# Kernel tuning notes

Measured on AMD Instinct MI355X. Metric: run time of the kernel, lower is better.

## Reference

```python
import jax, jax.numpy as jnp
import numpy as np

NUM_HEADS = 16
BLOCK_SIZE = 64
NUM_GLOBAL_TOKENS = 64
WINDOW_SIZE = 256
NUM_RANDOM_BLOCKS = 3
BATCH = 2
SEQ_LEN = 4096
EMBED_DIM = 1024


def _alibi_slopes(n):
    # power-of-2 head count path of _compute_alibi_slopes
    base = 2.0 ** (-(2.0 ** (-(np.log2(n) - 3.0))))
    return jnp.asarray([base ** i for i in range(1, n + 1)], dtype=jnp.float32)


def _build_block_indices():
    nb = SEQ_LEN // BLOCK_SIZE
    ngb = NUM_GLOBAL_TOKENS // BLOCK_SIZE
    wb = WINDOW_SIZE // BLOCK_SIZE
    mb = 2 * wb + 1 + NUM_RANDOM_BLOCKS
    rng = np.random.default_rng(0)
    out = np.full((nb, mb), -1, dtype=np.int64)
    for qb in range(nb):
        attended = set(range(ngb))  # global blocks handled separately
        idx = 0
        for kb in range(max(ngb, qb - wb), min(nb, qb + wb + 1)):
            if kb not in attended:
                out[qb, idx] = kb
                attended.add(kb)
                idx += 1
        cand = [b for b in range(ngb, nb) if b not in attended]
        pick = rng.choice(len(cand), size=min(NUM_RANDOM_BLOCKS, len(cand)), replace=False)
        for j in pick:
            out[qb, idx] = cand[j]
            idx += 1
    return jnp.asarray(out)


def setup_inputs() -> dict:
    key = jax.random.key(0)
    ks = jax.random.split(key, 5)
    s = 0.02
    x = jax.random.normal(ks[0], (BATCH, SEQ_LEN, EMBED_DIM), jnp.float32)
    Wq = jax.random.normal(ks[1], (EMBED_DIM, EMBED_DIM), jnp.float32) * s
    Wk = jax.random.normal(ks[2], (EMBED_DIM, EMBED_DIM), jnp.float32) * s
    Wv = jax.random.normal(ks[3], (EMBED_DIM, EMBED_DIM), jnp.float32) * s
    Wo = jax.random.normal(ks[4], (EMBED_DIM, EMBED_DIM), jnp.float32) * s
    return {"x": x, "Wq": Wq, "Wk": Wk, "Wv": Wv, "Wo": Wo,
            "block_indices": _build_block_indices()}


def reference(x, Wq, Wk, Wv, Wo, block_indices):
    B, S, E = x.shape
    H = NUM_HEADS
    Dh = E // H
    G = NUM_GLOBAL_TOKENS
    BS = BLOCK_SIZE
    scale = 1.0 / np.sqrt(Dh)

    def split_heads(t):
        return t.reshape(B, S, H, Dh).transpose(0, 2, 1, 3)  # [B,H,S,Dh]

    q = split_heads(x @ Wq)
    k = split_heads(x @ Wk)
    v = split_heads(x @ Wv)

    slopes = _alibi_slopes(H)  # [H]
    pos = jnp.arange(S, dtype=jnp.float32)

    # ---- global tokens: full attention over all keys ----
    sg = jnp.einsum('bhgd,bhsd->bhgs', q[:, :, :G], k) * scale
    bias_g = -slopes[:, None, None] * jnp.abs(pos[:G, None] - pos[None, :])  # [H,G,S]
    pg = jax.nn.softmax(sg + bias_g[None], axis=-1)
    out_g = jnp.einsum('bhgs,bhsd->bhgd', pg, v)  # [B,H,G,Dh]

    # ---- sparse queries: global KV + gathered sparse blocks ----
    nb = S // BS
    ngb = G // BS
    nqb = nb - ngb
    bi = block_indices[ngb:]           # [nqb, MB], -1 = padding
    mb = bi.shape[1]
    bsafe = jnp.maximum(bi, 0)

    kb = k.reshape(B, H, nb, BS, Dh)
    vb = v.reshape(B, H, nb, BS, Dh)
    kg = kb[:, :, bsafe].reshape(B, H, nqb, mb * BS, Dh)
    vg = vb[:, :, bsafe].reshape(B, H, nqb, mb * BS, Dh)
    kglob = jnp.broadcast_to(k[:, :, None, :G], (B, H, nqb, G, Dh))
    vglob = jnp.broadcast_to(v[:, :, None, :G], (B, H, nqb, G, Dh))
    kcat = jnp.concatenate([kglob, kg], axis=3)  # [B,H,nqb,G+mb*BS,Dh]
    vcat = jnp.concatenate([vglob, vg], axis=3)

    qn = q[:, :, G:].reshape(B, H, nqb, BS, Dh)
    scores = jnp.einsum('bhqmd,bhqnd->bhqmn', qn, kcat) * scale

    qpos = (G + jnp.arange(nqb * BS, dtype=jnp.float32)).reshape(nqb, BS)
    loc_pos = (bsafe[:, :, None] * BS + jnp.arange(BS)[None, None, :]).reshape(nqb, mb * BS).astype(jnp.float32)
    kpos = jnp.concatenate([jnp.broadcast_to(pos[:G][None], (nqb, G)), loc_pos], axis=1)
    bias = -slopes[:, None, None, None] * jnp.abs(qpos[None, :, :, None] - kpos[None, :, None, :])  # [H,nqb,BS,Kt]

    valid = jnp.concatenate([jnp.ones((nqb, G), bool), jnp.repeat(bi >= 0, BS, axis=1)], axis=1)
    scores = jnp.where(valid[None, None, :, None, :], scores + bias[None], -jnp.inf)
    p = jax.nn.softmax(scores, axis=-1)
    out_s = jnp.einsum('bhqmn,bhqnd->bhqmd', p, vcat).reshape(B, H, S - G, Dh)

    out = jnp.concatenate([out_g, out_s], axis=2)  # [B,H,S,Dh]
    out = out.transpose(0, 2, 1, 3).reshape(B, S, E)
    return out @ Wo
```

## Files before the change

### kernel.cpp

```cpp
#include <hip/hip_runtime.h>
#include <stdint.h>

typedef __attribute__((ext_vector_type(8))) short short8;
typedef __attribute__((ext_vector_type(4))) float f32x4;
typedef __attribute__((ext_vector_type(8))) unsigned short u16x8;
typedef __attribute__((ext_vector_type(2))) unsigned int u32x2;

#define DEV static __device__ __forceinline__

DEV unsigned short f2bf(float f) {
  union { float f; uint32_t u; } v; v.f = f;
  uint32_t r = v.u + 0x7FFFu + ((v.u >> 16) & 1u);
  return (unsigned short)(r >> 16);
}

DEV void gload16(const void* g, void* l) {
  __builtin_amdgcn_global_load_lds(
      (const __attribute__((address_space(1))) void*)g,
      (__attribute__((address_space(3))) void*)l, 16, 0, 0);
}

__global__ void cast_x_kernel(const float* __restrict__ x, unsigned short* __restrict__ xb) {
  int i = blockIdx.x * 256 + threadIdx.x;
  f32x4 a = ((const f32x4*)x)[2 * i];
  f32x4 b = ((const f32x4*)x)[2 * i + 1];
  u16x8 o;
  o[0] = f2bf(a[0]); o[1] = f2bf(a[1]); o[2] = f2bf(a[2]); o[3] = f2bf(a[3]);
  o[4] = f2bf(b[0]); o[5] = f2bf(b[1]); o[6] = f2bf(b[2]); o[7] = f2bf(b[3]);
  ((u16x8*)xb)[i] = o;
}

__global__ void transpose_w_kernel(const float* __restrict__ Wq, const float* __restrict__ Wk,
                                   const float* __restrict__ Wv, const float* __restrict__ Wo,
                                   unsigned short* __restrict__ wt) {
  __shared__ float tile[64][65];
  int z = blockIdx.z;
  const float* W = (z == 0) ? Wq : (z == 1) ? Wk : (z == 2) ? Wv : Wo;
  unsigned short* dst = wt + (size_t)z * 1024 * 1024;
  int bn = blockIdx.x, bk = blockIdx.y;
  int t = threadIdx.x;
  int c = t & 63, rr = t >> 6;
#pragma unroll
  for (int p = 0; p < 16; ++p) {
    int r = p * 4 + rr;
    tile[r][c] = W[(size_t)(bk * 64 + r) * 1024 + bn * 64 + c];
  }
  __syncthreads();
#pragma unroll
  for (int p = 0; p < 16; ++p) {
    int r2 = p * 4 + rr;
    dst[(size_t)(bn * 64 + r2) * 1024 + bk * 64 + c] = f2bf(tile[c][r2]);
  }
}

__global__ __launch_bounds__(256, 2) void gemm_qkv(const unsigned short* __restrict__ A,
                                                   const unsigned short* __restrict__ wt,
                                                   unsigned short* __restrict__ Qb,
                                                   unsigned short* __restrict__ Kb,
                                                   unsigned short* __restrict__ Vtb,
                                                   float qscale) {
  constexpr int K = 1024;
  __shared__ __align__(16) unsigned short As[2][128 * 64];
  __shared__ __align__(16) unsigned short Bs[2][128 * 64];
  int flat = blockIdx.x + 24 * blockIdx.y;
  int xcd = flat & 7, idx = flat >> 3;
  int bm = xcd * 8 + (idx & 7);
  int bn = idx >> 3;
  int which = bn >> 3, bnn = bn & 7;
  int tid = threadIdx.x, lane = tid & 63, w = tid >> 6;
  int wr = w >> 1, wc = w & 1;
  f32x4 acc[4][4] = {};

  int sr[4], soff[4];
#pragma unroll
  for (int i = 0; i < 4; ++i) {
    int ci = w * 4 + i;
    int r = ci * 8 + (lane >> 3);
    sr[i] = r;
    soff[i] = ((lane & 7) ^ (r & 7)) * 8;
  }
  const unsigned short* Arow = A + (size_t)(bm * 128) * K;
  const unsigned short* Brow = wt + (size_t)which * 1048576 + (size_t)(bnn * 128) * K;

  auto STAGE = [&](int bi, int k0) {
#pragma unroll
    for (int i = 0; i < 4; ++i) {
      gload16(Arow + (size_t)sr[i] * K + k0 + soff[i], &As[bi][(w * 4 + i) * 512]);
      gload16(Brow + (size_t)sr[i] * K + k0 + soff[i], &Bs[bi][(w * 4 + i) * 512]);
    }
  };

  STAGE(0, 0);
  for (int kt = 0; kt < 16; ++kt) {
    int cur = kt & 1;
    if (kt < 15) {
      STAGE(cur ^ 1, (kt + 1) * 64);
      asm volatile("s_waitcnt vmcnt(8)" ::: "memory");
    } else {
      asm volatile("s_waitcnt vmcnt(0)" ::: "memory");
    }
    __builtin_amdgcn_s_barrier();
    __builtin_amdgcn_sched_barrier(0);
    short8 af[2][4], bfr[2][4];
#pragma unroll
    for (int c = 0; c < 2; ++c) {
#pragma unroll
      for (int m = 0; m < 4; ++m) {
        int cc = (lane >> 4) + 4 * c;
        int ra = wr * 64 + m * 16 + (lane & 15);
        af[c][m] = *(const short8*)(&As[cur][ra * 64 + ((cc ^ (ra & 7)) * 8)]);
        int rb = wc * 64 + m * 16 + (lane & 15);
        bfr[c][m] = *(const short8*)(&Bs[cur][rb * 64 + ((cc ^ (rb & 7)) * 8)]);
      }
    }
#pragma unroll
    for (int c = 0; c < 2; ++c)
#pragma unroll
      for (int m = 0; m < 4; ++m)
#pragma unroll
        for (int n = 0; n < 4; ++n)
          acc[m][n] = __builtin_amdgcn_mfma_f32_16x16x32_bf16(af[c][m], bfr[c][n], acc[m][n], 0, 0, 0);
    __builtin_amdgcn_s_barrier();
    __builtin_amdgcn_sched_barrier(0);
  }

  int rbase = bm * 128 + wr * 64;
  int cbase = bnn * 128 + wc * 64;
#pragma unroll
  for (int m = 0; m < 4; ++m)
#pragma unroll
    for (int n = 0; n < 4; ++n) {
      int row0 = rbase + m * 16 + (lane >> 4) * 4;
      int col = cbase + n * 16 + (lane & 15);
      int h = col >> 6, d = col & 63;
      int b = row0 >> 12, s0 = row0 & 4095;
      if (which == 0) {
#pragma unroll
        for (int reg = 0; reg < 4; ++reg)
          Qb[((size_t)(b * 16 + h) * 4096 + s0 + reg) * 64 + d] = f2bf(acc[m][n][reg] * qscale);
      } else if (which == 1) {
#pragma unroll
        for (int reg = 0; reg < 4; ++reg)
          Kb[((size_t)(b * 16 + h) * 4096 + s0 + reg) * 64 + d] = f2bf(acc[m][n][reg]);
      } else {
        u32x2 pk;
        asm("v_cvt_pk_bf16_f32 %0, %1, %2" : "=v"(pk[0]) : "v"(acc[m][n][0]), "v"(acc[m][n][1]));
        asm("v_cvt_pk_bf16_f32 %0, %1, %2" : "=v"(pk[1]) : "v"(acc[m][n][2]), "v"(acc[m][n][3]));
        *(u32x2*)(Vtb + ((((size_t)(b * 16 + h) * 64 + (s0 >> 6)) * 64 + d) * 64 + (s0 & 63))) = pk;
      }
    }
}

__global__ __launch_bounds__(256, 2) void gemm_out(const unsigned short* __restrict__ A,
                                                   const unsigned short* __restrict__ Bt,
                                                   float* __restrict__ dst) {
  constexpr int K = 1024;
  __shared__ __align__(16) unsigned short As[2][128 * 64];
  __shared__ __align__(16) unsigned short Bs[2][128 * 64];
  int flat = blockIdx.x + 8 * blockIdx.y;
  int xcd = flat & 7, idx = flat >> 3;
  int bm = xcd * 8 + (idx & 7);
  int bn = idx >> 3;
  int tid = threadIdx.x, lane = tid & 63, w = tid >> 6;
  int wr = w >> 1, wc = w & 1;
  f32x4 acc[4][4] = {};

  int sr[4], soff[4];
#pragma unroll
  for (int i = 0; i < 4; ++i) {
    int ci = w * 4 + i;
    int r = ci * 8 + (lane >> 3);
    sr[i] = r;
    soff[i] = ((lane & 7) ^ (r & 7)) * 8;
  }
  const unsigned short* Arow = A + (size_t)(bm * 128) * K;
  const unsigned short* Brow = Bt + (size_t)(bn * 128) * K;

  auto STAGE = [&](int bi, int k0) {
#pragma unroll
    for (int i = 0; i < 4; ++i) {
      gload16(Arow + (size_t)sr[i] * K + k0 + soff[i], &As[bi][(w * 4 + i) * 512]);
      gload16(Brow + (size_t)sr[i] * K + k0 + soff[i], &Bs[bi][(w * 4 + i) * 512]);
    }
  };

  STAGE(0, 0);
  for (int kt = 0; kt < 16; ++kt) {
    int cur = kt & 1;
    if (kt < 15) {
      STAGE(cur ^ 1, (kt + 1) * 64);
      asm volatile("s_waitcnt vmcnt(8)" ::: "memory");
    } else {
      asm volatile("s_waitcnt vmcnt(0)" ::: "memory");
    }
    __builtin_amdgcn_s_barrier();
    __builtin_amdgcn_sched_barrier(0);
    short8 af[2][4], bfr[2][4];
#pragma unroll
    for (int c = 0; c < 2; ++c) {
#pragma unroll
      for (int m = 0; m < 4; ++m) {
        int cc = (lane >> 4) + 4 * c;
        int ra = wr * 64 + m * 16 + (lane & 15);
        af[c][m] = *(const short8*)(&As[cur][ra * 64 + ((cc ^ (ra & 7)) * 8)]);
        int rb = wc * 64 + m * 16 + (lane & 15);
        bfr[c][m] = *(const short8*)(&Bs[cur][rb * 64 + ((cc ^ (rb & 7)) * 8)]);
      }
    }
#pragma unroll
    for (int c = 0; c < 2; ++c)
#pragma unroll
      for (int m = 0; m < 4; ++m)
#pragma unroll
        for (int n = 0; n < 4; ++n)
          acc[m][n] = __builtin_amdgcn_mfma_f32_16x16x32_bf16(af[c][m], bfr[c][n], acc[m][n], 0, 0, 0);
    __builtin_amdgcn_s_barrier();
    __builtin_amdgcn_sched_barrier(0);
  }

  int rbase = bm * 128 + wr * 64;
  int cbase = bn * 128 + wc * 64;
#pragma unroll
  for (int m = 0; m < 4; ++m)
#pragma unroll
    for (int n = 0; n < 4; ++n) {
      int row0 = rbase + m * 16 + (lane >> 4) * 4;
      int col = cbase + n * 16 + (lane & 15);
#pragma unroll
      for (int reg = 0; reg < 4; ++reg)
        dst[(size_t)(row0 + reg) * 1024 + col] = acc[m][n][reg];
    }
}

__global__ __launch_bounds__(256) void attn_kernel(const unsigned short* __restrict__ Qh,
                            const unsigned short* __restrict__ Kh,
                            const unsigned short* __restrict__ Vbt,
                            const int* __restrict__ bidx,
                            unsigned short* __restrict__ attn_out,
                            float* __restrict__ Opart,
                            float* __restrict__ lpart) {
  __shared__ __align__(16) unsigned short Ks[3][64 * 64];
  __shared__ __align__(16) unsigned short Vs[2][64 * 64];
  int flat = blockIdx.x + 71 * blockIdx.y;
  int nf = (flat & 7) * 284 + (flat >> 3);
  int gx = nf % 71, bh = nf / 71;
  int h = bh & 15;
  int tid = threadIdx.x, lane = tid & 63, w = tid >> 6;
  int q = lane & 15, g = lane >> 4;
  float slope2 = exp2f(-0.5f * (float)(h + 1)) * 1.44269504f;

  int qb, nkb;
  int vlist;
  if (gx < 63) {
    qb = gx + 1;
    int v = -1;
    if (lane == 0) v = 0;
    else if (lane <= 12) v = bidx[qb * 12 + (lane - 1)];
    vlist = v;
    unsigned long long msk = __ballot(v >= 0);
    nkb = __builtin_popcountll(msk & 0x1FFFull);
  } else {
    qb = 0;
    nkb = 8;
    vlist = (gx - 63) * 8 + lane;
  }

  int qrow = qb * 64 + w * 16 + q;
  const unsigned short* qptr = Qh + ((size_t)bh * 4096 + qrow) * 64 + g * 8;
  short8 qf0 = *(const short8*)qptr;
  short8 qf1 = *(const short8*)(qptr + 32);

  float qposf = (float)qrow;
  float sq = slope2 * qposf;
  float er[4][4];
#pragma unroll
  for (int ct = 0; ct < 4; ++ct)
#pragma unroll
    for (int r = 0; r < 4; ++r) er[ct][r] = slope2 * (float)(ct * 16 + r);

  float psum = 0.f;
  f32x4 accO[4] = {};

  const unsigned short* Kbh = Kh + (size_t)bh * 4096 * 64;
  const unsigned short* Vbh = Vbt + (size_t)bh * 4096 * 64;

  int srr[2], so[2];
#pragma unroll
  for (int i = 0; i < 2; ++i) {
    int ci = w * 2 + i;
    int r = ci * 8 + (lane >> 3);
    srr[i] = r;
    so[i] = ((lane & 7) ^ (r & 7)) * 8;
  }
  auto STAGE_K = [&](int bi, int kb) {
    const unsigned short* kbase = Kbh + (size_t)kb * 4096;
#pragma unroll
    for (int i = 0; i < 2; ++i)
      gload16(kbase + srr[i] * 64 + so[i], &Ks[bi][(w * 2 + i) * 512]);
  };
  auto STAGE_V = [&](int bi, int kb) {
    const unsigned short* vbase = Vbh + (size_t)kb * 4096;
#pragma unroll
    for (int i = 0; i < 2; ++i)
      gload16(vbase + srr[i] * 64 + so[i], &Vs[bi][(w * 2 + i) * 512]);
  };

  STAGE_K(0, __builtin_amdgcn_readlane(vlist, 0));
  STAGE_V(0, __builtin_amdgcn_readlane(vlist, 0));
  STAGE_K(1, __builtin_amdgcn_readlane(vlist, 1));

  for (int it = 0; it < nkb; ++it) {
    int curK = it % 3, curV = it & 1;
    int kb = __builtin_amdgcn_readlane(vlist, it);
    if (it + 1 < nkb) {
      asm volatile("s_waitcnt vmcnt(2)" ::: "memory");
    } else {
      asm volatile("s_waitcnt vmcnt(0)" ::: "memory");
    }
    __builtin_amdgcn_s_barrier();
    __builtin_amdgcn_sched_barrier(0);
    if (it + 1 < nkb) STAGE_V((it + 1) & 1, __builtin_amdgcn_readlane(vlist, it + 1));
    if (it + 2 < nkb) STAGE_K((it + 2) % 3, __builtin_amdgcn_readlane(vlist, it + 2));

    float kb4g = (float)(kb * 64 + 4 * g);
    float d_[4][4];
    if (kb != qb) {
      if (kb < qb) {
        float t = __builtin_fmaf(slope2, kb4g, -sq);
#pragma unroll
        for (int ct = 0; ct < 4; ++ct)
#pragma unroll
          for (int r = 0; r < 4; ++r) d_[ct][r] = t + er[ct][r];
      } else {
        float t = sq - slope2 * kb4g;
#pragma unroll
        for (int ct = 0; ct < 4; ++ct)
#pragma unroll
          for (int r = 0; r < 4; ++r) d_[ct][r] = t - er[ct][r];
      }
    } else {
      float db = qposf - kb4g;
#pragma unroll
      for (int ct = 0; ct < 4; ++ct)
#pragma unroll
        for (int r = 0; r < 4; ++r)
          d_[ct][r] = -slope2 * fabsf(db - (float)(ct * 16 + r));
    }

    float pv[4][4];
    __builtin_amdgcn_s_setprio(1);
#pragma unroll
    for (int ct = 0; ct < 4; ++ct) {
      int kr = ct * 16 + q;
      short8 kf0 = *(const short8*)(&Ks[curK][kr * 64 + ((g ^ (kr & 7)) * 8)]);
      short8 kf1 = *(const short8*)(&Ks[curK][kr * 64 + (((g + 4) ^ (kr & 7)) * 8)]);
      f32x4 cin = {d_[ct][0], d_[ct][1], d_[ct][2], d_[ct][3]};
      f32x4 s = __builtin_amdgcn_mfma_f32_16x16x32_bf16(kf0, qf0, cin, 0, 0, 0);
      s = __builtin_amdgcn_mfma_f32_16x16x32_bf16(kf1, qf1, s, 0, 0, 0);
#pragma unroll
      for (int r = 0; r < 4; ++r) {
        float p = exp2f(s[r]);
        pv[ct][r] = p;
        psum += p;
      }
    }
    __builtin_amdgcn_s_setprio(0);

    uint32_t pkw[4][2];
#pragma unroll
    for (int ct = 0; ct < 4; ++ct) {
      asm("v_cvt_pk_bf16_f32 %0, %1, %2" : "=v"(pkw[ct][0]) : "v"(pv[ct][0]), "v"(pv[ct][1]));
      asm("v_cvt_pk_bf16_f32 %0, %1, %2" : "=v"(pkw[ct][1]) : "v"(pv[ct][2]), "v"(pv[ct][3]));
    }
    bool odd = (tid & 16) != 0;
    short8 pa[2];
#pragma unroll
    for (int f = 0; f < 2; ++f) {
      uint32_t s0 = pkw[2 * f][0], s1 = pkw[2 * f][1];
      uint32_t t0 = pkw[2 * f + 1][0], t1 = pkw[2 * f + 1][1];
      asm("v_permlane32_swap_b32 %0, %1" : "+v"(s0), "+v"(t0));
      asm("v_permlane32_swap_b32 %0, %1" : "+v"(s1), "+v"(t1));
      uint32_t xs0 = (uint32_t)__shfl_xor((int)s0, 16, 64);
      uint32_t xs1 = (uint32_t)__shfl_xor((int)s1, 16, 64);
      uint32_t xt0 = (uint32_t)__shfl_xor((int)t0, 16, 64);
      uint32_t xt1 = (uint32_t)__shfl_xor((int)t1, 16, 64);
      union { uint32_t w[4]; short8 v; } u;
      u.w[0] = odd ? xt0 : s0;
      u.w[1] = odd ? xt1 : s1;
      u.w[2] = odd ? t0 : xs0;
      u.w[3] = odd ? t1 : xs1;
      pa[f] = u.v;
    }

    __builtin_amdgcn_s_setprio(1);
#pragma unroll
    for (int dt = 0; dt < 4; ++dt) {
      int dr = dt * 16 + q;
      short8 vf0 = *(const short8*)(&Vs[curV][dr * 64 + ((g ^ (dr & 7)) * 8)]);
      short8 vf1 = *(const short8*)(&Vs[curV][dr * 64 + (((g + 4) ^ (dr & 7)) * 8)]);
      accO[dt] = __builtin_amdgcn_mfma_f32_16x16x32_bf16(pa[0], vf0, accO[dt], 0, 0, 0);
      accO[dt] = __builtin_amdgcn_mfma_f32_16x16x32_bf16(pa[1], vf1, accO[dt], 0, 0, 0);
    }
    __builtin_amdgcn_s_setprio(0);
  }

  float lt = psum;
  lt += __shfl_xor(lt, 16, 64);
  lt += __shfl_xor(lt, 32, 64);

  int b = bh >> 4;
  if (gx < 63) {
#pragma unroll
    for (int reg = 0; reg < 4; ++reg) {
      float ls = __shfl(lt, 4 * g + reg, 64);
      float rl = 1.0f / ls;
      int row = qb * 64 + w * 16 + 4 * g + reg;
#pragma unroll
      for (int dt = 0; dt < 4; ++dt) {
        int col = h * 64 + dt * 16 + q;
        attn_out[((size_t)b * 4096 + row) * 1024 + col] = f2bf(accO[dt][reg] * rl);
      }
    }
  } else {
    int chunk = gx - 63;
    float* Op = Opart + (size_t)(bh * 8 + chunk) * 64 * 64;
    float* lp = lpart + (size_t)(bh * 8 + chunk) * 64;
#pragma unroll
    for (int reg = 0; reg < 4; ++reg) {
      int row = w * 16 + 4 * g + reg;
#pragma unroll
      for (int dt = 0; dt < 4; ++dt) {
        int col = dt * 16 + q;
        Op[row * 64 + col] = accO[dt][reg];
      }
    }
    if (g == 0) lp[w * 16 + q] = lt;
  }
}

__global__ void merge_qb0(const float* __restrict__ Opart, const float* __restrict__ lpart,
                          unsigned short* __restrict__ attn_out) {
  int bh = blockIdx.x;
  int tid = threadIdx.x;
  int row = tid >> 2, cg = tid & 3;
  const float* lp = lpart + (size_t)bh * 8 * 64;
  float L = 0.f;
#pragma unroll
  for (int c = 0; c < 8; ++c) L += lp[c * 64 + row];
  float rL = 1.0f / L;
  int b = bh >> 4, h = bh & 15;
  f32x4 acc0 = {}, acc1 = {}, acc2 = {}, acc3 = {};
#pragma unroll
  for (int c = 0; c < 8; ++c) {
    const float* Op = Opart + ((size_t)(bh * 8 + c) * 64 + row) * 64 + cg * 16;
    acc0 += ((const f32x4*)Op)[0];
    acc1 += ((const f32x4*)Op)[1];
    acc2 += ((const f32x4*)Op)[2];
    acc3 += ((const f32x4*)Op)[3];
  }
  unsigned short* out = attn_out + ((size_t)b * 4096 + row) * 1024 + h * 64 + cg * 16;
#pragma unroll
  for (int j = 0; j < 4; ++j) {
    out[j] = f2bf(acc0[j] * rL);
    out[4 + j] = f2bf(acc1[j] * rL);
    out[8 + j] = f2bf(acc2[j] * rL);
    out[12 + j] = f2bf(acc3[j] * rL);
  }
}

extern "C" void kernel_launch(void* const* d_in, const int* in_sizes, int n_in,
                              void* d_out, int out_size, void* d_ws, size_t ws_size,
                              hipStream_t stream) {
  const float* x = (const float*)d_in[0];
  const float* Wq = (const float*)d_in[1];
  const float* Wk = (const float*)d_in[2];
  const float* Wv = (const float*)d_in[3];
  const float* Wo = (const float*)d_in[4];
  const int* bidx = (const int*)d_in[5];

  char* ws = (char*)d_ws;
  unsigned short* xb = (unsigned short*)(ws);
  unsigned short* wt = (unsigned short*)(ws + 16777216);
  unsigned short* Qb = (unsigned short*)(ws + 25165824);
  unsigned short* Kb = (unsigned short*)(ws + 41943040);
  unsigned short* Vtb = (unsigned short*)(ws + 58720256);
  unsigned short* attnb = (unsigned short*)(ws + 75497472);
  float* Opart = (float*)(ws);
  float* lpart = (float*)(ws + 4194304);

  cast_x_kernel<<<4096, 256, 0, stream>>>(x, xb);
  transpose_w_kernel<<<dim3(16, 16, 4), 256, 0, stream>>>(Wq, Wk, Wv, Wo, wt);
  gemm_qkv<<<dim3(24, 64), 256, 0, stream>>>(xb, wt, Qb, Kb, Vtb, 0.18033688f);
  attn_kernel<<<dim3(71, 32), 256, 0, stream>>>(Qb, Kb, Vtb, bidx, attnb, Opart, lpart);
  merge_qb0<<<32, 256, 0, stream>>>(Opart, lpart, attnb);
  gemm_out<<<dim3(8, 64), 256, 0, stream>>>(attnb, wt + 3145728, (float*)d_out);
}
```

Before: 165.5 us.

## Merge cast and weight transpose into one prep kernel; single-barrier GEMM pipeline

The x-to-bf16 cast and the weight transpose/cast are folded into a single launch, with blocks branching on blockIdx, which saves one kernel launch and its drain gap. In both GEMM kernels the double-buffered loop now waits for all loads, hits one barrier, and only then issues the prefetch for the next tile, dropping the second barrier per iteration. The prefetch still overlaps the MFMA compute. Because the wait is now vmcnt(0) and the next load is issued only after the barrier, load latency may be exposed more than with the earlier vmcnt(8) scheme.

```diff
diff --git a/kernel.cpp b/kernel.cpp
--- a/kernel.cpp
+++ b/kernel.cpp
@@ -20,25 +20,29 @@
       (__attribute__((address_space(3))) void*)l, 16, 0, 0);
 }
 
-__global__ void cast_x_kernel(const float* __restrict__ x, unsigned short* __restrict__ xb) {
-  int i = blockIdx.x * 256 + threadIdx.x;
-  f32x4 a = ((const f32x4*)x)[2 * i];
-  f32x4 b = ((const f32x4*)x)[2 * i + 1];
-  u16x8 o;
-  o[0] = f2bf(a[0]); o[1] = f2bf(a[1]); o[2] = f2bf(a[2]); o[3] = f2bf(a[3]);
-  o[4] = f2bf(b[0]); o[5] = f2bf(b[1]); o[6] = f2bf(b[2]); o[7] = f2bf(b[3]);
-  ((u16x8*)xb)[i] = o;
-}
-
-__global__ void transpose_w_kernel(const float* __restrict__ Wq, const float* __restrict__ Wk,
-                                   const float* __restrict__ Wv, const float* __restrict__ Wo,
-                                   unsigned short* __restrict__ wt) {
+__global__ __launch_bounds__(256) void prep_kernel(const float* __restrict__ x,
+                                                   unsigned short* __restrict__ xb,
+                                                   const float* __restrict__ Wq,
+                                                   const float* __restrict__ Wk,
+                                                   const float* __restrict__ Wv,
+                                                   const float* __restrict__ Wo,
+                                                   unsigned short* __restrict__ wt) {
   __shared__ float tile[64][65];
-  int z = blockIdx.z;
+  int t = threadIdx.x;
+  if (blockIdx.x < 4096) {
+    int i = blockIdx.x * 256 + t;
+    f32x4 a = ((const f32x4*)x)[2 * i];
+    f32x4 b = ((const f32x4*)x)[2 * i + 1];
+    u16x8 o;
+    o[0] = f2bf(a[0]); o[1] = f2bf(a[1]); o[2] = f2bf(a[2]); o[3] = f2bf(a[3]);
+    o[4] = f2bf(b[0]); o[5] = f2bf(b[1]); o[6] = f2bf(b[2]); o[7] = f2bf(b[3]);
+    ((u16x8*)xb)[i] = o;
+    return;
+  }
+  int flat = blockIdx.x - 4096;
+  int bn = flat & 15, bk = (flat >> 4) & 15, z = flat >> 8;
   const float* W = (z == 0) ? Wq : (z == 1) ? Wk : (z == 2) ? Wv : Wo;
   unsigned short* dst = wt + (size_t)z * 1024 * 1024;
-  int bn = blockIdx.x, bk = blockIdx.y;
-  int t = threadIdx.x;
   int c = t & 63, rr = t >> 6;
 #pragma unroll
   for (int p = 0; p < 16; ++p) {
@@ -93,13 +97,10 @@
   STAGE(0, 0);
   for (int kt = 0; kt < 16; ++kt) {
     int cur = kt & 1;
-    if (kt < 15) {
-      STAGE(cur ^ 1, (kt + 1) * 64);
-      asm volatile("s_waitcnt vmcnt(8)" ::: "memory");
-    } else {
-      asm volatile("s_waitcnt vmcnt(0)" ::: "memory");
-    }
+    asm volatile("s_waitcnt vmcnt(0)" ::: "memory");
     __builtin_amdgcn_s_barrier();
+    __builtin_amdgcn_sched_barrier(0);
+    if (kt < 15) STAGE(cur ^ 1, (kt + 1) * 64);
     __builtin_amdgcn_sched_barrier(0);
     short8 af[2][4], bfr[2][4];
 #pragma unroll
@@ -120,8 +121,6 @@
 #pragma unroll
         for (int n = 0; n < 4; ++n)
           acc[m][n] = __builtin_amdgcn_mfma_f32_16x16x32_bf16(af[c][m], bfr[c][n], acc[m][n], 0, 0, 0);
-    __builtin_amdgcn_s_barrier();
-    __builtin_amdgcn_sched_barrier(0);
   }
 
   int rbase = bm * 128 + wr * 64;
@@ -187,13 +186,10 @@
   STAGE(0, 0);
   for (int kt = 0; kt < 16; ++kt) {
     int cur = kt & 1;
-    if (kt < 15) {
-      STAGE(cur ^ 1, (kt + 1) * 64);
-      asm volatile("s_waitcnt vmcnt(8)" ::: "memory");
-    } else {
-      asm volatile("s_waitcnt vmcnt(0)" ::: "memory");
-    }
+    asm volatile("s_waitcnt vmcnt(0)" ::: "memory");
     __builtin_amdgcn_s_barrier();
+    __builtin_amdgcn_sched_barrier(0);
+    if (kt < 15) STAGE(cur ^ 1, (kt + 1) * 64);
     __builtin_amdgcn_sched_barrier(0);
     short8 af[2][4], bfr[2][4];
 #pragma unroll
@@ -214,8 +210,6 @@
 #pragma unroll
         for (int n = 0; n < 4; ++n)
           acc[m][n] = __builtin_amdgcn_mfma_f32_16x16x32_bf16(af[c][m], bfr[c][n], acc[m][n], 0, 0, 0);
-    __builtin_amdgcn_s_barrier();
-    __builtin_amdgcn_sched_barrier(0);
   }
 
   int rbase = bm * 128 + wr * 64;
@@ -488,8 +482,7 @@
   float* Opart = (float*)(ws);
   float* lpart = (float*)(ws + 4194304);
 
-  cast_x_kernel<<<4096, 256, 0, stream>>>(x, xb);
-  transpose_w_kernel<<<dim3(16, 16, 4), 256, 0, stream>>>(Wq, Wk, Wv, Wo, wt);
+  prep_kernel<<<5120, 256, 0, stream>>>(x, xb, Wq, Wk, Wv, Wo, wt);
   gemm_qkv<<<dim3(24, 64), 256, 0, stream>>>(xb, wt, Qb, Kb, Vtb, 0.18033688f);
   attn_kernel<<<dim3(71, 32), 256, 0, stream>>>(Qb, Kb, Vtb, bidx, attnb, Opart, lpart);
   merge_qb0<<<32, 256, 0, stream>>>(Opart, lpart, attnb);
```

Result: no change. 165.5 us (+0.0%).
